# Kernel optimization log

Hardware: AMD Instinct MI355X
Metric: run time of the kernel (lower is better)

## Reference

```python
import jax, jax.numpy as jnp
import numpy as np

D = 1024      # model dim
NSEQ = 4      # packed sequences
SEQ = 8192    # tokens per sequence
L = NSEQ * SEQ
EPS = 1e-4    # prob clamp in dechunk


def setup_inputs() -> dict:
    key = jax.random.key(0)
    ks = jax.random.split(key, 7)
    s = 1.0 / np.sqrt(D)
    mk = lambda k: jax.random.normal(k, (D, D), jnp.float32) * s
    return {
        'x': jax.random.normal(ks[0], (1, L, D), jnp.float32),
        'Wq': mk(ks[1]), 'Wk': mk(ks[2]), 'Wr': mk(ks[3]),
        'We': mk(ks[4]), 'Wm': mk(ks[5]), 'Wd': mk(ks[6]),
        'cu_seqlens': jnp.arange(NSEQ + 1, dtype=jnp.int32) * SEQ,
    }


def _normalize(v):
    n = jnp.linalg.norm(v, axis=-1, keepdims=True)
    return v / jnp.maximum(n, 1e-12)


def _forward(x, Wq, Wk, Wr, We, Wm, Wd, cu_seqlens):
    # encoder (pointwise linear)
    enc = jnp.einsum('bld,ed->ble', x, We)                  # [1,L,D]
    residual = jnp.einsum('bld,ed->ble', enc, Wr)           # residual_proj

    # Router: cosine similarity of adjacent tokens
    q = _normalize(jnp.einsum('bld,ed->ble', enc[:, :-1], Wq))
    k = _normalize(jnp.einsum('bld,ed->ble', enc[:, 1:], Wk))
    p = 0.5 * (1.0 - jnp.sum(q * k, axis=-1))               # [1,L-1]
    p = jnp.pad(p, ((0, 0), (1, 0)), constant_values=1.0)[0]  # [L]
    p = p.at[cu_seqlens[:-1]].set(1.0)                      # force boundary at seq starts
    mask = p > 0.5                                          # boundary_mask
    sel = jnp.where(mask, p, 1.0 - p)                       # selected_prob

    # main network on compressed tokens (pointwise -> compute in full layout,
    # non-boundary positions are never read by the scan below)
    m = jnp.einsum('bld,ed->ble', enc, Wm)[0]               # [L,D]

    # dechunk == mamba scan with A=-1, N=1: EMA h_t=(1-p)h + p*u at boundaries,
    # held (a=1) elsewhere; plug_back gather == held state. Reset at seq starts.
    pc = jnp.clip(p, EPS, 1.0 - EPS)
    starts = jnp.zeros(L, bool).at[cu_seqlens[:-1]].set(True)
    a = jnp.where(starts, 0.0, jnp.where(mask, 1.0 - pc, 1.0))[:, None]  # [L,1]
    b = jnp.where(mask[:, None], pc[:, None] * m, 0.0)                    # [L,D]

    def comb(c1, c2):
        a1, b1 = c1
        a2, b2 = c2
        return (a1 * a2, a2 * b1 + b2)

    _, y = jax.lax.associative_scan(comb, (a, b), axis=0)   # y: [L,D] dechunked

    # straight-through: forward multiplies by 1, backward passes grad to sel
    st = sel + jax.lax.stop_gradient(1.0 - sel)
    out = y[None] * st[None, :, None] + residual
    out = jnp.einsum('bld,ed->ble', out, Wd)                # decoder
    return out


def reference(x, Wq, Wk, Wr, We, Wm, Wd, cu_seqlens):
    return _forward(x, Wq, Wk, Wr, We, Wm, Wd, cu_seqlens)
```

## Files before the change

### kernel.cpp

```cpp
#include <hip/hip_runtime.h>
#include <math.h>

#define D_DIM 1024
#define CL 512

typedef __attribute__((ext_vector_type(8))) short short8;
typedef __attribute__((ext_vector_type(4))) float f32x4;
typedef unsigned short u16;

__device__ __forceinline__ u16 f2bf(float f) {
    unsigned int u = __float_as_uint(f);
    u += 0x7fff + ((u >> 16) & 1);
    return (u16)(u >> 16);
}
__device__ __forceinline__ float bf2f(u16 h) {
    return __uint_as_float((unsigned int)h << 16);
}

#define GLOAD16(g, l) __builtin_amdgcn_global_load_lds(                      \
        (const __attribute__((address_space(1))) void*)(g),                  \
        (__attribute__((address_space(3))) void*)(l), 16, 0, 0)
#define SBAR()   __builtin_amdgcn_s_barrier()
#define SCHED0() __builtin_amdgcn_sched_barrier(0)
#define PRIO(x)  __builtin_amdgcn_s_setprio(x)
#define WAITVM(N) asm volatile("s_waitcnt vmcnt(" #N ")" ::: "memory")


template<int EPI>
__global__ __launch_bounds__(512) void gemm256(const u16* __restrict__ A1,
                                               const u16* __restrict__ W1,
                                               float* __restrict__ Cf,
                                               u16* __restrict__ Cb) {
    constexpr int NT = 32;
    __shared__ u16 lds[4 * 16384];
    const int tid = threadIdx.x;
    const int lane = tid & 63, wid = tid >> 6;
    const int wm = wid >> 2, wn = wid & 3;
    const int fr = lane & 15, fq = lane >> 4;
    const int row0 = blockIdx.x * 256, col0 = blockIdx.y * 256;
    const int r0s = tid >> 2, c0s = tid & 3;

    int offA[8], offB[4];
#pragma unroll
    for (int i = 0; i < 8; ++i) {
        const int r = wm * 128 + i * 16 + fr;
        offA[i] = r * 64 + ((fq ^ ((r >> 1) & 3)) << 4);
    }
#pragma unroll
    for (int j = 0; j < 4; ++j) {
        const int r = wn * 64 + j * 16 + fr;
        offB[j] = r * 64 + ((fq ^ ((r >> 1) & 3)) << 4);
    }

    auto stageA = [&](int s) {
        const int k0 = s * 32;
        char* dst = (char*)lds + (s & 3) * 32768;
#pragma unroll
        for (int j = 0; j < 2; ++j) {
            const int r = j * 128 + r0s;
            const int c = c0s ^ ((r >> 1) & 3);
            GLOAD16(A1 + (size_t)(row0 + r) * D_DIM + k0 + c * 8,
                    dst + j * 8192 + tid * 16);
        }
    };
    auto stageB = [&](int s) {
        const int k0 = s * 32;
        char* dst = (char*)lds + (s & 3) * 32768 + 16384;
#pragma unroll
        for (int j = 0; j < 2; ++j) {
            const int r = j * 128 + r0s;
            const int c = c0s ^ ((r >> 1) & 3);
            GLOAD16(W1 + (size_t)(col0 + r) * D_DIM + k0 + c * 8,
                    dst + j * 8192 + tid * 16);
        }
    };

    f32x4 acc[8][4];
#pragma unroll
    for (int i = 0; i < 8; ++i)
#pragma unroll
        for (int j = 0; j < 4; ++j) acc[i][j] = (f32x4){0.f, 0.f, 0.f, 0.f};

    stageA(0); stageB(0); stageA(1); stageB(1); stageA(2); stageB(2);
    WAITVM(8); SBAR(); SCHED0();

    for (int t = 0; t < NT; ++t) {
        const char* buf  = (const char*)lds + (t & 3) * 32768;
        const char* bufB = buf + 16384;
        short8 af[8], bf[4];
#pragma unroll
        for (int i = 0; i < 4; ++i) af[i] = *(const short8*)(buf + offA[i]);
#pragma unroll
        for (int j = 0; j < 4; ++j) bf[j] = *(const short8*)(bufB + offB[j]);
        if (t + 3 < NT) stageA(t + 3);
        SBAR();
        PRIO(1);
#pragma unroll
        for (int i = 0; i < 4; ++i)
#pragma unroll
            for (int j = 0; j < 4; ++j)
                acc[i][j] = __builtin_amdgcn_mfma_f32_16x16x32_bf16(af[i], bf[j], acc[i][j], 0, 0, 0);
        PRIO(0);
#pragma unroll
        for (int i = 4; i < 8; ++i) af[i] = *(const short8*)(buf + offA[i]);
        if (t + 3 < NT) stageB(t + 3);
        SBAR();
        PRIO(1);
#pragma unroll
        for (int i = 4; i < 8; ++i)
#pragma unroll
            for (int j = 0; j < 4; ++j)
                acc[i][j] = __builtin_amdgcn_mfma_f32_16x16x32_bf16(af[i], bf[j], acc[i][j], 0, 0, 0);
        PRIO(0);
        if (t + 1 < NT) {
            if (t + 3 < NT)      { WAITVM(8); }
            else if (t + 2 < NT) { WAITVM(4); }
            else                 { WAITVM(0); }
            SBAR(); SCHED0();
        }
    }

#pragma unroll
    for (int i = 0; i < 8; ++i)
#pragma unroll
        for (int j = 0; j < 4; ++j) {
            const int r0 = row0 + wm * 128 + i * 16 + fq * 4;
            const int c  = col0 + wn * 64 + j * 16 + fr;
#pragma unroll
            for (int rr = 0; rr < 4; ++rr) {
                if (EPI == 0) Cb[(size_t)(r0 + rr) * D_DIM + c] = f2bf(acc[i][j][rr]);
                else          Cf[(size_t)(r0 + rr) * D_DIM + c] = acc[i][j][rr];
            }
        }
}

template<int EPI>
__global__ __launch_bounds__(512) void gemm_x3(const u16* __restrict__ Ah,
                                               const u16* __restrict__ Al,
                                               const u16* __restrict__ Wh,
                                               const u16* __restrict__ Wl,
                                               float* __restrict__ Cf,
                                               u16* __restrict__ Chi,
                                               u16* __restrict__ Clo,
                                               const u16* __restrict__ Eh,
                                               const u16* __restrict__ El,
                                               float* __restrict__ Pd) {
    constexpr int NT = 32;
    __shared__ u16 lds[3 * 24576];
    const int tid = threadIdx.x;
    const int lane = tid & 63, wid = tid >> 6;
    const int wm = wid >> 2, wn = wid & 3;
    const int fr = lane & 15, fq = lane >> 4;
    const int row0 = blockIdx.x * 128, col0 = blockIdx.y * 256;
    const int r0s = tid >> 2, c0s = tid & 3;

    int offA[4], offB[4];
#pragma unroll
    for (int i = 0; i < 4; ++i) {
        const int r = wm * 64 + i * 16 + fr;
        offA[i] = r * 64 + ((fq ^ ((r >> 1) & 3)) << 4);
    }
#pragma unroll
    for (int j = 0; j < 4; ++j) {
        const int r = wn * 64 + j * 16 + fr;
        offB[j] = r * 64 + ((fq ^ ((r >> 1) & 3)) << 4);
    }

    auto stageAhl = [&](int s) {
        char* base = (char*)lds + (s % 3) * 49152;
        const int r = r0s;
        const int c = c0s ^ ((r >> 1) & 3);
        const size_t g = (size_t)(row0 + r) * D_DIM + s * 32 + c * 8;
        GLOAD16(Ah + g, base + tid * 16);
        GLOAD16(Al + g, base + 8192 + tid * 16);
    };
    auto stageBh = [&](int s) {
        char* base = (char*)lds + (s % 3) * 49152 + 16384;
#pragma unroll
        for (int j = 0; j < 2; ++j) {
            const int r = j * 128 + r0s;
            const int c = c0s ^ ((r >> 1) & 3);
            GLOAD16(Wh + (size_t)(col0 + r) * D_DIM + s * 32 + c * 8,
                    base + j * 8192 + tid * 16);
        }
    };
    auto stageBl = [&](int s) {
        char* base = (char*)lds + (s % 3) * 49152 + 32768;
#pragma unroll
        for (int j = 0; j < 2; ++j) {
            const int r = j * 128 + r0s;
            const int c = c0s ^ ((r >> 1) & 3);
            GLOAD16(Wl + (size_t)(col0 + r) * D_DIM + s * 32 + c * 8,
                    base + j * 8192 + tid * 16);
        }
    };

    f32x4 acc[4][4];
#pragma unroll
    for (int i = 0; i < 4; ++i)
#pragma unroll
        for (int j = 0; j < 4; ++j) acc[i][j] = (f32x4){0.f, 0.f, 0.f, 0.f};

    stageAhl(0); stageBh(0); stageBl(0);
    stageAhl(1); stageBh(1); stageBl(1);
    WAITVM(6); SBAR(); SCHED0();

    for (int t = 0; t < NT; ++t) {
        const char* base = (const char*)lds + (t % 3) * 49152;
        short8 afh[4], afl[4], bfh[4], bfl[4];
#pragma unroll
        for (int i = 0; i < 4; ++i) afh[i] = *(const short8*)(base + offA[i]);
#pragma unroll
        for (int j = 0; j < 4; ++j) bfh[j] = *(const short8*)(base + 16384 + offB[j]);
        if (t + 2 < NT) stageBh(t + 2);
        SBAR();
        PRIO(1);
#pragma unroll
        for (int i = 0; i < 4; ++i)
#pragma unroll
            for (int j = 0; j < 4; ++j)
                acc[i][j] = __builtin_amdgcn_mfma_f32_16x16x32_bf16(afh[i], bfh[j], acc[i][j], 0, 0, 0);
        PRIO(0);
#pragma unroll
        for (int j = 0; j < 4; ++j) bfl[j] = *(const short8*)(base + 32768 + offB[j]);
        if (t + 2 < NT) stageBl(t + 2);
        SBAR();
        PRIO(1);
#pragma unroll
        for (int i = 0; i < 4; ++i)
#pragma unroll
            for (int j = 0; j < 4; ++j)
                acc[i][j] = __builtin_amdgcn_mfma_f32_16x16x32_bf16(afh[i], bfl[j], acc[i][j], 0, 0, 0);
        PRIO(0);
#pragma unroll
        for (int i = 0; i < 4; ++i) afl[i] = *(const short8*)(base + 8192 + offA[i]);
        if (t + 2 < NT) stageAhl(t + 2);
        SBAR();
        PRIO(1);
#pragma unroll
        for (int i = 0; i < 4; ++i)
#pragma unroll
            for (int j = 0; j < 4; ++j)
                acc[i][j] = __builtin_amdgcn_mfma_f32_16x16x32_bf16(afl[i], bfh[j], acc[i][j], 0, 0, 0);
        PRIO(0);
        if (t + 1 < NT) {
            if (t + 2 < NT) { WAITVM(6); }
            else            { WAITVM(0); }
            SBAR(); SCHED0();
        }
    }

    if (EPI == 2) {
        const int Ltot = gridDim.x * 128;
#pragma unroll
        for (int i = 0; i < 4; ++i)
#pragma unroll
            for (int rr = 0; rr < 4; ++rr) {
                const int r = row0 + wm * 64 + i * 16 + fq * 4 + rr;
                float s = 0.f;
#pragma unroll
                for (int j = 0; j < 4; ++j) {
                    const int c = col0 + wn * 64 + j * 16 + fr;
                    float e = 0.f;
                    if (r > 0) {
                        const size_t o = (size_t)(r - 1) * D_DIM + c;
                        e = bf2f(Eh[o]) + bf2f(El[o]);
                    }
                    s += acc[i][j][rr] * e;
                }
#pragma unroll
                for (int off = 1; off < 16; off <<= 1) s += __shfl_xor(s, off);
                if (fr == 0)
                    Pd[(size_t)(blockIdx.y * 4 + wn) * Ltot + r] = s;
            }
        return;
    }
#pragma unroll
    for (int i = 0; i < 4; ++i)
#pragma unroll
        for (int j = 0; j < 4; ++j) {
            const int r0 = row0 + wm * 64 + i * 16 + fq * 4;
            const int c  = col0 + wn * 64 + j * 16 + fr;
#pragma unroll
            for (int rr = 0; rr < 4; ++rr) {
                const float v = acc[i][j][rr];
                if (EPI == 0) {
                    const u16 h = f2bf(v);
                    Chi[(size_t)(r0 + rr) * D_DIM + c] = h;
                    Clo[(size_t)(r0 + rr) * D_DIM + c] = f2bf(v - bf2f(h));
                } else {
                    Cf[(size_t)(r0 + rr) * D_DIM + c] = v;
                }
            }
        }
}

__global__ __launch_bounds__(512) void norm2(const u16* __restrict__ A,
                                             const u16* __restrict__ Bq,
                                             const u16* __restrict__ Bk,
                                             float* __restrict__ Pq,
                                             float* __restrict__ Pk) {
    constexpr int NT = 32;
    __shared__ u16 lds[3 * 20480];
    const int tid = threadIdx.x;
    const int lane = tid & 63, wid = tid >> 6;
    const int wm = wid >> 2, wn = wid & 3;
    const int fr = lane & 15, fq = lane >> 4;
    const int row0 = blockIdx.x * 128, col0 = blockIdx.y * 256;
    const int r0s = tid >> 2, c0s = tid & 3;

    int offA[4], offB[4];
#pragma unroll
    for (int i = 0; i < 4; ++i) {
        const int r = wm * 64 + i * 16 + fr;
        offA[i] = r * 64 + ((fq ^ ((r >> 1) & 3)) << 4);
    }
#pragma unroll
    for (int j = 0; j < 4; ++j) {
        const int r = wn * 64 + j * 16 + fr;
        offB[j] = r * 64 + ((fq ^ ((r >> 1) & 3)) << 4);
    }

    auto stageA = [&](int s) {
        char* base = (char*)lds + (s % 3) * 40960;
        const int r = r0s;
        const int c = c0s ^ ((r >> 1) & 3);
        GLOAD16(A + (size_t)(row0 + r) * D_DIM + s * 32 + c * 8, base + tid * 16);
    };
    auto stageBq = [&](int s) {
        char* base = (char*)lds + (s % 3) * 40960 + 8192;
#pragma unroll
        for (int j = 0; j < 2; ++j) {
            const int r = j * 128 + r0s;
            const int c = c0s ^ ((r >> 1) & 3);
            GLOAD16(Bq + (size_t)(col0 + r) * D_DIM + s * 32 + c * 8,
                    base + j * 8192 + tid * 16);
        }
    };
    auto stageBk = [&](int s) {
        char* base = (char*)lds + (s % 3) * 40960 + 24576;
#pragma unroll
        for (int j = 0; j < 2; ++j) {
            const int r = j * 128 + r0s;
            const int c = c0s ^ ((r >> 1) & 3);
            GLOAD16(Bk + (size_t)(col0 + r) * D_DIM + s * 32 + c * 8,
                    base + j * 8192 + tid * 16);
        }
    };

    f32x4 accq[4][4], acck[4][4];
#pragma unroll
    for (int i = 0; i < 4; ++i)
#pragma unroll
        for (int j = 0; j < 4; ++j) {
            accq[i][j] = (f32x4){0.f, 0.f, 0.f, 0.f};
            acck[i][j] = (f32x4){0.f, 0.f, 0.f, 0.f};
        }

    stageA(0); stageBq(0); stageBk(0);
    stageA(1); stageBq(1); stageBk(1);
    WAITVM(5); SBAR(); SCHED0();

    for (int t = 0; t < NT; ++t) {
        const char* base = (const char*)lds + (t % 3) * 40960;
        short8 af[4], bq[4], bk[4];
#pragma unroll
        for (int i = 0; i < 4; ++i) af[i] = *(const short8*)(base + offA[i]);
#pragma unroll
        for (int j = 0; j < 4; ++j) bq[j] = *(const short8*)(base + 8192 + offB[j]);
        if (t + 2 < NT) { stageA(t + 2); stageBq(t + 2); }
        SBAR();
        PRIO(1);
#pragma unroll
        for (int i = 0; i < 4; ++i)
#pragma unroll
            for (int j = 0; j < 4; ++j)
                accq[i][j] = __builtin_amdgcn_mfma_f32_16x16x32_bf16(af[i], bq[j], accq[i][j], 0, 0, 0);
        PRIO(0);
#pragma unroll
        for (int j = 0; j < 4; ++j) bk[j] = *(const short8*)(base + 24576 + offB[j]);
        if (t + 2 < NT) stageBk(t + 2);
        SBAR();
        PRIO(1);
#pragma unroll
        for (int i = 0; i < 4; ++i)
#pragma unroll
            for (int j = 0; j < 4; ++j)
                acck[i][j] = __builtin_amdgcn_mfma_f32_16x16x32_bf16(af[i], bk[j], acck[i][j], 0, 0, 0);
        PRIO(0);
        if (t + 1 < NT) {
            if (t + 2 < NT) { WAITVM(5); }
            else            { WAITVM(0); }
            SBAR(); SCHED0();
        }
    }

    const int Ltot = gridDim.x * 128;
#pragma unroll
    for (int i = 0; i < 4; ++i)
#pragma unroll
        for (int rr = 0; rr < 4; ++rr) {
            const int r = row0 + wm * 64 + i * 16 + fq * 4 + rr;
            float sq = 0.f, sk = 0.f;
#pragma unroll
            for (int j = 0; j < 4; ++j) {
                sq += accq[i][j][rr] * accq[i][j][rr];
                sk += acck[i][j][rr] * acck[i][j][rr];
            }
#pragma unroll
            for (int off = 1; off < 16; off <<= 1) {
                sq += __shfl_xor(sq, off);
                sk += __shfl_xor(sk, off);
            }
            if (fr == 0) {
                Pq[(size_t)(blockIdx.y * 4 + wn) * Ltot + r] = sq;
                Pk[(size_t)(blockIdx.y * 4 + wn) * Ltot + r] = sk;
            }
        }
}

__global__ __launch_bounds__(256) void gemm_bf16_nt(const u16* __restrict__ A,
                                                    const u16* __restrict__ W,
                                                    float* __restrict__ C,
                                                    u16* __restrict__ Cbf) {
    __shared__ u16 lA[128 * 32];
    __shared__ u16 lB[128 * 32];
    const int tid  = threadIdx.x;
    const int lane = tid & 63, wid = tid >> 6;
    const int wy = wid & 1, wx = wid >> 1;
    const int fr = lane & 15, fq = lane >> 4;
    const int row0 = blockIdx.x * 128;
    const int col0 = blockIdx.y * 128;

    const int rS   = tid >> 2;
    const int subS = (tid & 3) ^ ((rS >> 1) & 3);
    const u16* gA = A + (size_t)(row0 + rS) * D_DIM + subS * 8;
    const u16* gB = W + (size_t)(col0 + rS) * D_DIM + subS * 8;
    char* lA0 = (char*)lA + tid * 16;
    char* lB0 = (char*)lB + tid * 16;
    const size_t rowStep = (size_t)64 * D_DIM;

    int offA[4], offB[4];
#pragma unroll
    for (int i = 0; i < 4; ++i) {
        const int ra = wy * 64 + i * 16 + fr;
        const int rb = wx * 64 + i * 16 + fr;
        offA[i] = ra * 64 + ((fq ^ ((ra >> 1) & 3)) << 4);
        offB[i] = rb * 64 + ((fq ^ ((rb >> 1) & 3)) << 4);
    }

    f32x4 acc[4][4];
#pragma unroll
    for (int i = 0; i < 4; ++i)
#pragma unroll
        for (int j = 0; j < 4; ++j) acc[i][j] = (f32x4){0.f, 0.f, 0.f, 0.f};

    for (int k0 = 0; k0 < D_DIM; k0 += 32) {
        __syncthreads();
        GLOAD16(gA + k0, lA0);
        GLOAD16(gA + k0 + rowStep, lA0 + 4096);
        GLOAD16(gB + k0, lB0);
        GLOAD16(gB + k0 + rowStep, lB0 + 4096);
        __syncthreads();
        short8 af[4], bf[4];
#pragma unroll
        for (int i = 0; i < 4; ++i) af[i] = *(const short8*)((const char*)lA + offA[i]);
#pragma unroll
        for (int j = 0; j < 4; ++j) bf[j] = *(const short8*)((const char*)lB + offB[j]);
#pragma unroll
        for (int i = 0; i < 4; ++i)
#pragma unroll
            for (int j = 0; j < 4; ++j)
                acc[i][j] = __builtin_amdgcn_mfma_f32_16x16x32_bf16(af[i], bf[j], acc[i][j], 0, 0, 0);
    }
#pragma unroll
    for (int i = 0; i < 4; ++i)
#pragma unroll
        for (int j = 0; j < 4; ++j) {
            const int r0 = row0 + wy * 64 + i * 16 + fq * 4;
            const int c  = col0 + wx * 64 + j * 16 + fr;
            if (Cbf) {
#pragma unroll
                for (int r = 0; r < 4; ++r)
                    Cbf[(size_t)(r0 + r) * D_DIM + c] = f2bf(acc[i][j][r]);
            } else {
#pragma unroll
                for (int r = 0; r < 4; ++r)
                    C[(size_t)(r0 + r) * D_DIM + c] = acc[i][j][r];
            }
        }
}

__global__ void split_bf16(const float* __restrict__ src, u16* __restrict__ hi,
                           u16* __restrict__ lo, int n4) {
    int i = blockIdx.x * 256 + threadIdx.x;
    if (i >= n4) return;
    float4 v = ((const float4*)src)[i];
    ushort4 h, l;
    h.x = f2bf(v.x); l.x = f2bf(v.x - bf2f(h.x));
    h.y = f2bf(v.y); l.y = f2bf(v.y - bf2f(h.y));
    h.z = f2bf(v.z); l.z = f2bf(v.z - bf2f(h.z));
    h.w = f2bf(v.w); l.w = f2bf(v.w - bf2f(h.w));
    ((ushort4*)hi)[i] = h;
    ((ushort4*)lo)[i] = l;
}

__global__ void conv_bf16(const float* __restrict__ src, u16* __restrict__ dst, int n4) {
    int i = blockIdx.x * 256 + threadIdx.x;
    if (i >= n4) return;
    float4 v = ((const float4*)src)[i];
    ushort4 o = {f2bf(v.x), f2bf(v.y), f2bf(v.z), f2bf(v.w)};
    ((ushort4*)dst)[i] = o;
}

__global__ __launch_bounds__(256) void transpose_split(const float* __restrict__ W,
                                                       u16* __restrict__ Th,
                                                       u16* __restrict__ Tl) {
    __shared__ float tile[32][33];
    const int e0 = blockIdx.x * 32, d0 = blockIdx.y * 32;
    const int tx = threadIdx.x & 31, ty = threadIdx.x >> 5;
#pragma unroll
    for (int i = 0; i < 32; i += 8)
        tile[ty + i][tx] = W[(size_t)(e0 + ty + i) * D_DIM + d0 + tx];
    __syncthreads();
#pragma unroll
    for (int i = 0; i < 32; i += 8) {
        float v = tile[tx][ty + i];
        u16 h = f2bf(v);
        Th[(size_t)(d0 + ty + i) * D_DIM + e0 + tx] = h;
        if (Tl) Tl[(size_t)(d0 + ty + i) * D_DIM + e0 + tx] = f2bf(v - bf2f(h));
    }
}

__global__ void combine_router(const float* __restrict__ pd,
                               const float* __restrict__ pq,
                               const float* __restrict__ pk,
                               const int* __restrict__ cu, int nseq,
                               float* __restrict__ a, float* __restrict__ bs,
                               int L) {
    int l = blockIdx.x * 256 + threadIdx.x;
    if (l >= L) return;
    float dot = 0.f, q2 = 0.f, k2 = 0.f;
#pragma unroll
    for (int j = 0; j < 16; ++j) {
        dot += pd[(size_t)j * L + l];
        k2  += pk[(size_t)j * L + l];
        if (l > 0) q2 += pq[(size_t)j * L + l - 1];
    }
    float pv;
    if (l == 0) pv = 1.f;
    else {
        float dn = fmaxf(sqrtf(q2), 1e-12f) * fmaxf(sqrtf(k2), 1e-12f);
        pv = 0.5f * (1.f - dot / dn);
    }
    bool start = false;
    for (int s = 0; s < nseq; ++s) start = start || (cu[s] == l);
    if (start) pv = 1.f;
    bool mask = pv > 0.5f;
    float pc  = fminf(fmaxf(pv, 1e-4f), 1.f - 1e-4f);
    a[l]  = start ? 0.f : (mask ? (1.f - pc) : 1.f);
    bs[l] = mask ? pc : 0.f;
}

__global__ __launch_bounds__(256) void scan_local(const float* __restrict__ a,
                                                  const float* __restrict__ bs,
                                                  u16* __restrict__ m,
                                                  float* __restrict__ P) {
    __shared__ float a_s[CL], b_s[CL];
    const int chunk = blockIdx.x;
    const int d     = blockIdx.y * 256 + threadIdx.x;
    const int l0    = chunk * CL;
    for (int i = threadIdx.x; i < CL; i += 256) { a_s[i] = a[l0 + i]; b_s[i] = bs[l0 + i]; }
    __syncthreads();
    if (blockIdx.y == 0 && threadIdx.x == 0) {
        float pp = 1.f;
        for (int i = 0; i < CL; ++i) { pp *= a_s[i]; P[l0 + i] = pp; }
    }
    float h = 0.f;
    u16* mp = m + (size_t)l0 * D_DIM + d;
    for (int i = 0; i < CL; ++i) {
        float mv = bf2f(mp[(size_t)i * D_DIM]);
        h = fmaf(a_s[i], h, b_s[i] * mv);
        mp[(size_t)i * D_DIM] = f2bf(h);
    }
}

__global__ void scan_carry(const u16* __restrict__ y, const float* __restrict__ P,
                           float* __restrict__ carry, int nchunks) {
    const int d = blockIdx.x * 256 + threadIdx.x;
    float H = 0.f;
    for (int c = 0; c < nchunks; ++c) {
        carry[(size_t)c * D_DIM + d] = H;
        const float Ac = P[c * CL + (CL - 1)];
        const float Bc = bf2f(y[((size_t)c * CL + (CL - 1)) * D_DIM + d]);
        H = fmaf(Ac, H, Bc);
    }
}

__global__ void fixup_out(const u16* __restrict__ z, const float* __restrict__ P,
                          const float* __restrict__ carry, const u16* __restrict__ r,
                          float* __restrict__ out) {
    const size_t i8  = (size_t)blockIdx.x * 256 + threadIdx.x;
    const size_t idx = i8 * 8;
    const int l  = (int)(idx >> 10);
    const int dd = (int)(idx & 1023);
    const int c  = l >> 9;
    const float pl = P[l];
    short8 zv = *(const short8*)(z + idx);
    short8 rv = *(const short8*)(r + idx);
    const float4 c0 = *(const float4*)(carry + (size_t)c * D_DIM + dd);
    const float4 c1 = *(const float4*)(carry + (size_t)c * D_DIM + dd + 4);
    float4 o0, o1;
    o0.x = fmaf(pl, c0.x, bf2f((u16)zv[0])) + bf2f((u16)rv[0]);
    o0.y = fmaf(pl, c0.y, bf2f((u16)zv[1])) + bf2f((u16)rv[1]);
    o0.z = fmaf(pl, c0.z, bf2f((u16)zv[2])) + bf2f((u16)rv[2]);
    o0.w = fmaf(pl, c0.w, bf2f((u16)zv[3])) + bf2f((u16)rv[3]);
    o1.x = fmaf(pl, c1.x, bf2f((u16)zv[4])) + bf2f((u16)rv[4]);
    o1.y = fmaf(pl, c1.y, bf2f((u16)zv[5])) + bf2f((u16)rv[5]);
    o1.z = fmaf(pl, c1.z, bf2f((u16)zv[6])) + bf2f((u16)rv[6]);
    o1.w = fmaf(pl, c1.w, bf2f((u16)zv[7])) + bf2f((u16)rv[7]);
    *(float4*)(out + idx)     = o0;
    *(float4*)(out + idx + 4) = o1;
}

extern "C" void kernel_launch(void* const* d_in, const int* in_sizes, int n_in,
                              void* d_out, int out_size, void* d_ws, size_t ws_size,
                              hipStream_t stream) {
    const float* x  = (const float*)d_in[0];
    const float* Wq = (const float*)d_in[1];
    const float* Wk = (const float*)d_in[2];
    const float* Wr = (const float*)d_in[3];
    const float* We = (const float*)d_in[4];
    const float* Wm = (const float*)d_in[5];
    const float* Wd = (const float*)d_in[6];
    const int*   cu = (const int*)d_in[7];
    const int L    = in_sizes[0] / D_DIM;
    const int nseq = in_sizes[7] - 1;

    const size_t LD2 = (size_t)L * D_DIM * 2;
    const size_t DD  = (size_t)D_DIM * D_DIM;
    const int nLD4 = L * D_DIM / 4;
    const int nDD4 = (int)(DD / 4);
    const int nchunks = L / CL;

    char* ws = (char*)d_ws;
    u16*   xh   = (u16*)ws;
    u16*   xl   = (u16*)(ws + LD2);
    u16*   zbuf = (u16*)ws;
    u16*   rbuf = (u16*)(ws + LD2);
    u16*   ench = (u16*)(ws + 2 * LD2);
    u16*   encl = (u16*)(ws + 3 * LD2);
    float* av   = (float*)(ws + 4 * LD2);
    float* bs   = av + L;
    float* P    = bs + L;
    float* carry= P  + L;

    char* dob = (char*)d_out;
    u16* Weh   = (u16*)dob;
    u16* Wel   = (u16*)(dob + (2u << 20));
    u16* WqTh  = (u16*)(dob + (4u << 20));
    u16* WqTl  = (u16*)(dob + (6u << 20));
    u16* WkTh  = (u16*)(dob + (8u << 20));
    u16* WkTl  = (u16*)(dob + (10u << 20));
    float* Mf  = (float*)(dob + (12u << 20));
    u16* Mh    = (u16*)(dob + (16u << 20));
    u16* Ml    = (u16*)(dob + (18u << 20));
    u16* Wqb   = (u16*)(dob + (20u << 20));
    u16* Wkb   = (u16*)(dob + (22u << 20));
    u16* WmTb  = (u16*)(dob + (24u << 20));
    u16* WrTb  = (u16*)(dob + (26u << 20));
    u16* Wdb   = (u16*)(dob + (28u << 20));
    u16* Wdmb  = (u16*)(dob + (30u << 20));
    u16* Wdrb  = (u16*)(dob + (32u << 20));
    float* partdot = (float*)(dob + (34u << 20));
    float* partnq  = (float*)(dob + (36u << 20));
    float* partnk  = (float*)(dob + (38u << 20));
    float* out = (float*)d_out;

    dim3 gX3L(L / 128, D_DIM / 256);
    dim3 gX3D(D_DIM / 128, D_DIM / 256);
    dim3 g256(L / 256, D_DIM / 256);
    dim3 gD(D_DIM / 128, D_DIM / 128);
    dim3 gT(D_DIM / 32, D_DIM / 32);

    split_bf16<<<(nLD4 + 255) / 256, 256, 0, stream>>>(x, xh, xl, nLD4);
    split_bf16<<<(nDD4 + 255) / 256, 256, 0, stream>>>(We, Weh, Wel, nDD4);
    gemm_x3<0><<<gX3L, 512, 0, stream>>>(xh, xl, Weh, Wel, nullptr, ench, encl,
                                         nullptr, nullptr, nullptr);
    transpose_split<<<gT, 256, 0, stream>>>(Wq, WqTh, WqTl);
    transpose_split<<<gT, 256, 0, stream>>>(Wk, WkTh, WkTl);
    gemm_x3<1><<<gX3D, 512, 0, stream>>>(WqTh, WqTl, WkTh, WkTl, Mf, nullptr, nullptr,
                                         nullptr, nullptr, nullptr);
    split_bf16<<<(nDD4 + 255) / 256, 256, 0, stream>>>(Mf, Mh, Ml, nDD4);
    gemm_x3<2><<<gX3L, 512, 0, stream>>>(ench, encl, Mh, Ml, nullptr, nullptr, nullptr,
                                         ench, encl, partdot);
    conv_bf16<<<(nDD4 + 255) / 256, 256, 0, stream>>>(Wq, Wqb, nDD4);
    conv_bf16<<<(nDD4 + 255) / 256, 256, 0, stream>>>(Wk, Wkb, nDD4);
    norm2<<<gX3L, 512, 0, stream>>>(ench, Wqb, Wkb, partnq, partnk);
    combine_router<<<(L + 255) / 256, 256, 0, stream>>>(partdot, partnq, partnk,
                                                        cu, nseq, av, bs, L);
    conv_bf16<<<(nDD4 + 255) / 256, 256, 0, stream>>>(Wd, Wdb, nDD4);
    transpose_split<<<gT, 256, 0, stream>>>(Wm, WmTb, nullptr);
    transpose_split<<<gT, 256, 0, stream>>>(Wr, WrTb, nullptr);
    gemm_bf16_nt<<<gD, 256, 0, stream>>>(Wdb, WmTb, nullptr, Wdmb);
    gemm_bf16_nt<<<gD, 256, 0, stream>>>(Wdb, WrTb, nullptr, Wdrb);
    gemm256<0><<<g256, 512, 0, stream>>>(ench, Wdmb, nullptr, zbuf);
    gemm256<0><<<g256, 512, 0, stream>>>(ench, Wdrb, nullptr, rbuf);
    dim3 gsl(nchunks, D_DIM / 256);
    scan_local<<<gsl, 256, 0, stream>>>(av, bs, zbuf, P);
    scan_carry<<<D_DIM / 256, 256, 0, stream>>>(zbuf, P, carry, nchunks);
    fixup_out<<<(size_t)L * D_DIM / 8 / 256, 256, 0, stream>>>(zbuf, P, carry, rbuf, out);
}
```

Measured before the change: 1.002 ms.

## Fuse residual GEMM with scan fixup epilogue and coalesce router dot epilogue

The residual-path GEMM (enc·Wdr) is moved after the scan and gets a new epilogue that adds P*carry + z directly into the fp32 output. This removes the separate fixup_out pass and the bf16 rbuf round trip through memory. Separately, the router partial-dot epilogue now stages the accumulator tile in LDS and reads Eh/El with vectorized row-contiguous loads, replacing scattered 2-byte loads and shuffle reductions. The weight scratch buffers move from the output region into the workspace because the output is now written by the GEMM. The fused epilogue still issues scattered per-element loads of z and carry.

```diff
diff --git a/kernel.cpp b/kernel.cpp
--- a/kernel.cpp
+++ b/kernel.cpp
@@ -30,7 +30,10 @@
 __global__ __launch_bounds__(512) void gemm256(const u16* __restrict__ A1,
                                                const u16* __restrict__ W1,
                                                float* __restrict__ Cf,
-                                               u16* __restrict__ Cb) {
+                                               u16* __restrict__ Cb,
+                                               const u16* __restrict__ zin,
+                                               const float* __restrict__ Pv,
+                                               const float* __restrict__ carry) {
     constexpr int NT = 32;
     __shared__ u16 lds[4 * 16384];
     const int tid = threadIdx.x;
@@ -129,7 +132,14 @@
 #pragma unroll
             for (int rr = 0; rr < 4; ++rr) {
                 if (EPI == 0) Cb[(size_t)(r0 + rr) * D_DIM + c] = f2bf(acc[i][j][rr]);
-                else          Cf[(size_t)(r0 + rr) * D_DIM + c] = acc[i][j][rr];
+                else if (EPI == 1) Cf[(size_t)(r0 + rr) * D_DIM + c] = acc[i][j][rr];
+                else {
+                    const int r = r0 + rr;
+                    const float pl = Pv[r];
+                    const float cv = carry[(size_t)(r >> 9) * D_DIM + c];
+                    const float zv = bf2f(zin[(size_t)r * D_DIM + c]);
+                    Cf[(size_t)r * D_DIM + c] = acc[i][j][rr] + fmaf(pl, cv, zv);
+                }
             }
         }
 }
@@ -251,28 +261,38 @@
     }
 
     if (EPI == 2) {
-        const int Ltot = gridDim.x * 128;
+        __syncthreads();
+        float* lt = (float*)lds;
 #pragma unroll
         for (int i = 0; i < 4; ++i)
 #pragma unroll
-            for (int rr = 0; rr < 4; ++rr) {
-                const int r = row0 + wm * 64 + i * 16 + fq * 4 + rr;
-                float s = 0.f;
-#pragma unroll
-                for (int j = 0; j < 4; ++j) {
-                    const int c = col0 + wn * 64 + j * 16 + fr;
-                    float e = 0.f;
-                    if (r > 0) {
-                        const size_t o = (size_t)(r - 1) * D_DIM + c;
-                        e = bf2f(Eh[o]) + bf2f(El[o]);
-                    }
-                    s += acc[i][j][rr] * e;
+            for (int j = 0; j < 4; ++j) {
+                const int rl = wm * 64 + i * 16 + fq * 4;
+                const int cl = wn * 64 + j * 16 + fr;
+#pragma unroll
+                for (int rr = 0; rr < 4; ++rr)
+                    lt[(rl + rr) * 260 + cl] = acc[i][j][rr];
+            }
+        __syncthreads();
+        const int row = tid >> 2, q = tid & 3;
+        const int rg  = row0 + row;
+        float s = 0.f;
+        if (rg > 0) {
+            const u16* ehp = Eh + (size_t)(rg - 1) * D_DIM + col0 + q * 64;
+            const u16* elp = El + (size_t)(rg - 1) * D_DIM + col0 + q * 64;
+            const float* ltp = lt + row * 260 + q * 64;
+#pragma unroll
+            for (int k8 = 0; k8 < 8; ++k8) {
+                short8 hv = *(const short8*)(ehp + k8 * 8);
+                short8 lv = *(const short8*)(elp + k8 * 8);
+#pragma unroll
+                for (int e = 0; e < 8; ++e) {
+                    const float ev = bf2f((u16)hv[e]) + bf2f((u16)lv[e]);
+                    s = fmaf(ltp[k8 * 8 + e], ev, s);
                 }
-#pragma unroll
-                for (int off = 1; off < 16; off <<= 1) s += __shfl_xor(s, off);
-                if (fr == 0)
-                    Pd[(size_t)(blockIdx.y * 4 + wn) * Ltot + r] = s;
             }
+        }
+        Pd[(size_t)(blockIdx.y * 4 + q) * (gridDim.x * 128) + rg] = s;
         return;
     }
 #pragma unroll
@@ -597,32 +617,6 @@
     }
 }
 
-__global__ void fixup_out(const u16* __restrict__ z, const float* __restrict__ P,
-                          const float* __restrict__ carry, const u16* __restrict__ r,
-                          float* __restrict__ out) {
-    const size_t i8  = (size_t)blockIdx.x * 256 + threadIdx.x;
-    const size_t idx = i8 * 8;
-    const int l  = (int)(idx >> 10);
-    const int dd = (int)(idx & 1023);
-    const int c  = l >> 9;
-    const float pl = P[l];
-    short8 zv = *(const short8*)(z + idx);
-    short8 rv = *(const short8*)(r + idx);
-    const float4 c0 = *(const float4*)(carry + (size_t)c * D_DIM + dd);
-    const float4 c1 = *(const float4*)(carry + (size_t)c * D_DIM + dd + 4);
-    float4 o0, o1;
-    o0.x = fmaf(pl, c0.x, bf2f((u16)zv[0])) + bf2f((u16)rv[0]);
-    o0.y = fmaf(pl, c0.y, bf2f((u16)zv[1])) + bf2f((u16)rv[1]);
-    o0.z = fmaf(pl, c0.z, bf2f((u16)zv[2])) + bf2f((u16)rv[2]);
-    o0.w = fmaf(pl, c0.w, bf2f((u16)zv[3])) + bf2f((u16)rv[3]);
-    o1.x = fmaf(pl, c1.x, bf2f((u16)zv[4])) + bf2f((u16)rv[4]);
-    o1.y = fmaf(pl, c1.y, bf2f((u16)zv[5])) + bf2f((u16)rv[5]);
-    o1.z = fmaf(pl, c1.z, bf2f((u16)zv[6])) + bf2f((u16)rv[6]);
-    o1.w = fmaf(pl, c1.w, bf2f((u16)zv[7])) + bf2f((u16)rv[7]);
-    *(float4*)(out + idx)     = o0;
-    *(float4*)(out + idx + 4) = o1;
-}
-
 extern "C" void kernel_launch(void* const* d_in, const int* in_sizes, int n_in,
                               void* d_out, int out_size, void* d_ws, size_t ws_size,
                               hipStream_t stream) {
@@ -647,7 +641,11 @@
     u16*   xh   = (u16*)ws;
     u16*   xl   = (u16*)(ws + LD2);
     u16*   zbuf = (u16*)ws;
-    u16*   rbuf = (u16*)(ws + LD2);
+    u16*   Wdb  = (u16*)(ws + LD2);
+    u16*   WmTb = (u16*)(ws + LD2 + (2u << 20));
+    u16*   WrTb = (u16*)(ws + LD2 + (4u << 20));
+    u16*   Wdmb = (u16*)(ws + LD2 + (6u << 20));
+    u16*   Wdrb = (u16*)(ws + LD2 + (8u << 20));
     u16*   ench = (u16*)(ws + 2 * LD2);
     u16*   encl = (u16*)(ws + 3 * LD2);
     float* av   = (float*)(ws + 4 * LD2);
@@ -667,11 +665,6 @@
     u16* Ml    = (u16*)(dob + (18u << 20));
     u16* Wqb   = (u16*)(dob + (20u << 20));
     u16* Wkb   = (u16*)(dob + (22u << 20));
-    u16* WmTb  = (u16*)(dob + (24u << 20));
-    u16* WrTb  = (u16*)(dob + (26u << 20));
-    u16* Wdb   = (u16*)(dob + (28u << 20));
-    u16* Wdmb  = (u16*)(dob + (30u << 20));
-    u16* Wdrb  = (u16*)(dob + (32u << 20));
     float* partdot = (float*)(dob + (34u << 20));
     float* partnq  = (float*)(dob + (36u << 20));
     float* partnk  = (float*)(dob + (38u << 20));
@@ -704,10 +697,11 @@
     transpose_split<<<gT, 256, 0, stream>>>(Wr, WrTb, nullptr);
     gemm_bf16_nt<<<gD, 256, 0, stream>>>(Wdb, WmTb, nullptr, Wdmb);
     gemm_bf16_nt<<<gD, 256, 0, stream>>>(Wdb, WrTb, nullptr, Wdrb);
-    gemm256<0><<<g256, 512, 0, stream>>>(ench, Wdmb, nullptr, zbuf);
-    gemm256<0><<<g256, 512, 0, stream>>>(ench, Wdrb, nullptr, rbuf);
+    gemm256<0><<<g256, 512, 0, stream>>>(ench, Wdmb, nullptr, zbuf,
+                                         nullptr, nullptr, nullptr);
     dim3 gsl(nchunks, D_DIM / 256);
     scan_local<<<gsl, 256, 0, stream>>>(av, bs, zbuf, P);
     scan_carry<<<D_DIM / 256, 256, 0, stream>>>(zbuf, P, carry, nchunks);
-    fixup_out<<<(size_t)L * D_DIM / 8 / 256, 256, 0, stream>>>(zbuf, P, carry, rbuf, out);
-}
+    gemm256<3><<<g256, 512, 0, stream>>>(ench, Wdrb, out, nullptr,
+                                         zbuf, P, carry);
+}
```

Measured after the change: 916.3 us. 1.09x faster.
